# Optimization experiments

Measured on AMD Instinct MI355X. Metric: run time of the kernel, lower is better.

The kernel has to match this reference:

```python
import jax, jax.numpy as jnp
import numpy as np

N_NODES = 40000
N_EDGES = 640000
D_FEAT = 128
HIDDEN = 128
N_GRAPHS = 512


def setup_inputs() -> dict:
    key = jax.random.key(0)
    ks = jax.random.split(key, 6)
    x = jax.random.normal(ks[0], (N_NODES, D_FEAT), dtype=jnp.float32)
    edge_index = jax.random.randint(ks[1], (2, N_EDGES), 0, N_NODES, dtype=jnp.int32)
    batch = jnp.sort(jax.random.randint(ks[2], (N_NODES,), 0, N_GRAPHS, dtype=jnp.int32))
    s1 = 1.0 / np.sqrt(D_FEAT)
    s2 = 1.0 / np.sqrt(HIDDEN)
    W1 = jax.random.normal(ks[3], (D_FEAT, HIDDEN), dtype=jnp.float32) * s1
    b1 = jnp.zeros((HIDDEN,), dtype=jnp.float32)
    W2 = jax.random.normal(ks[4], (HIDDEN, HIDDEN), dtype=jnp.float32) * s2
    b2 = jnp.zeros((HIDDEN,), dtype=jnp.float32)
    Wfc = jax.random.normal(ks[5], (HIDDEN, 1), dtype=jnp.float32) * s2
    bfc = jnp.zeros((1,), dtype=jnp.float32)
    return {"x": x, "edge_index": edge_index, "batch": batch,
            "W1": W1, "b1": b1, "W2": W2, "b2": b2, "Wfc": Wfc, "bfc": bfc}


def _gcn_conv(x, edge_index, W, b):
    # PyG GCNConv: linear transform, add self-loops, symmetric deg^{-1/2} norm,
    # scatter-add messages from row (source) to col (target), then bias.
    n = x.shape[0]
    h = x @ W  # [N, H]
    row, col = edge_index[0], edge_index[1]
    ones = jnp.ones_like(col, dtype=h.dtype)
    deg = 1.0 + jax.ops.segment_sum(ones, col, num_segments=n)  # self-loop included
    dinv = jax.lax.rsqrt(deg)  # [N]
    norm = dinv[row] * dinv[col]  # [E]
    msg = h[row] * norm[:, None]  # [E, H]
    out = jax.ops.segment_sum(msg, col, num_segments=n)
    out = out + h * (dinv * dinv)[:, None]  # self-loop contribution
    return out + b


def _mean_pool(x, batch, num_graphs):
    sums = jax.ops.segment_sum(x, batch, num_segments=num_graphs)
    cnt = jax.ops.segment_sum(jnp.ones((x.shape[0],), dtype=x.dtype), batch, num_segments=num_graphs)
    return sums / jnp.maximum(cnt, 1.0)[:, None]


def reference(x, edge_index, batch, W1, b1, W2, b2, Wfc, bfc):
    h = jax.nn.relu(_gcn_conv(x, edge_index, W1, b1))
    h = jax.nn.relu(_gcn_conv(h, edge_index, W2, b2))
    g = _mean_pool(h, batch, N_GRAPHS)  # [G, H]
    return g @ Wfc + bfc  # [G, 1]
```

## Files before the change

kernel.cpp:

```cpp
#include <hip/hip_runtime.h>
#include <hip/hip_fp16.h>

#define N_NODES 40000
#define N_EDGES 640000
#define NFEAT   128
#define N_GRAPHS 512
#define SCAN_NB 157
#define EPAD_MAX (N_EDGES + 3 * N_NODES)


__global__ void edge_deg_int_kernel(const int* __restrict__ ei, int* __restrict__ degcnt, int E) {
    int e = blockIdx.x * blockDim.x + threadIdx.x;
    if (e < E) atomicAdd(&degcnt[ei[E + e]], 1);
}

__global__ void batch_hist_kernel(const int* __restrict__ batch, int* __restrict__ gcnt, int n) {
    int i = blockIdx.x * blockDim.x + threadIdx.x;
    if (i < n) atomicAdd(&gcnt[batch[i]], 1);
}

__global__ void dinv_from_int_kernel(const int* __restrict__ degcnt, float* __restrict__ dinv, int n) {
    int i = blockIdx.x * blockDim.x + threadIdx.x;
    if (i < n) dinv[i] = rsqrtf(1.0f + (float)degcnt[i]);
}

__global__ void scan1_kernel(const int* __restrict__ in, int* __restrict__ out,
                             int* __restrict__ bsums, float* __restrict__ dinv, int n) {
    __shared__ int tmp[256];
    int t = threadIdx.x;
    int i = blockIdx.x * 256 + t;
    int deg = (i < n) ? in[i] : 0;
    if (i < n) dinv[i] = rsqrtf(1.0f + (float)deg);
    int vp = (i < n) ? ((deg + 3) & ~3) : 0;
    tmp[t] = vp;
    __syncthreads();
    for (int off = 1; off < 256; off <<= 1) {
        int add = (t >= off) ? tmp[t - off] : 0;
        __syncthreads();
        tmp[t] += add;
        __syncthreads();
    }
    if (i < n) out[i] = tmp[t] - vp;
    if (t == 255) bsums[blockIdx.x] = tmp[255];
}

__global__ void scan2_kernel(int* __restrict__ bsums, int nb) {
    __shared__ int tmp[256];
    int t = threadIdx.x;
    int v = (t < nb) ? bsums[t] : 0;
    tmp[t] = v;
    __syncthreads();
    for (int off = 1; off < 256; off <<= 1) {
        int add = (t >= off) ? tmp[t - off] : 0;
        __syncthreads();
        tmp[t] += add;
        __syncthreads();
    }
    if (t < nb) bsums[t] = tmp[t] - v;
}

__global__ void scan3_kernel(int* __restrict__ rowptr, const int* __restrict__ bsums,
                             int* __restrict__ cursor, const int* __restrict__ degcnt,
                             int n) {
    int i = blockIdx.x * 256 + threadIdx.x;
    if (i < n) {
        int v = rowptr[i] + bsums[blockIdx.x];
        rowptr[i] = v;
        cursor[i] = v;
        if (i == n - 1) rowptr[n] = v + ((degcnt[i] + 3) & ~3);
    }
}

template <typename IdxT>
__global__ void fill_kernel(const int* __restrict__ ei, int* __restrict__ cursor,
                            IdxT* __restrict__ csr, int E) {
    int e = blockIdx.x * blockDim.x + threadIdx.x;
    if (e < E) {
        int c = ei[E + e];
        int p = atomicAdd(&cursor[c], 1);
        csr[p] = (IdxT)ei[e];
    }
}

template <typename IdxT>
__global__ void pad_kernel(const int* __restrict__ rowptr, const int* __restrict__ cursor,
                           IdxT* __restrict__ csr, int n) {
    int i = blockIdx.x * blockDim.x + threadIdx.x;
    if (i < n) {
        int end = rowptr[i + 1];
        for (int p = cursor[i]; p < end; ++p) csr[p] = (IdxT)N_NODES;
    }
}

__global__ void out_init_kernel(float* __restrict__ out, const float* __restrict__ bfc, int g) {
    int i = blockIdx.x * blockDim.x + threadIdx.x;
    if (i < g) out[i] = bfc[0];
}

template <typename OutT>
__global__ __launch_bounds__(256, 4) void gemm64_kernel(const float* __restrict__ X,
                                                        const float* __restrict__ W,
                                                        const float* __restrict__ dinv,
                                                        OutT* __restrict__ H) {
    __shared__ float Ws[128 * 64];
    const int colhalf = blockIdx.x & 1;
    const int tile    = blockIdx.x >> 1;

    for (int i = threadIdx.x; i < 2048; i += 256) {
        int k   = i >> 4;
        int cc4 = (i & 15) * 4;
        *(float4*)(Ws + k * 64 + cc4) = *(const float4*)(W + k * 128 + colhalf * 64 + cc4);
    }
    __syncthreads();

    const int rg = threadIdx.x >> 4;
    const int cg = threadIdx.x & 15;
    const int row0 = tile * 64 + rg * 4;
    const float* x0 = X + (size_t)row0 * NFEAT;

    float acc[4][4] = {};
    float4 xc[4], xn[4];
    #pragma unroll
    for (int i = 0; i < 4; i++) xc[i] = *(const float4*)(x0 + (size_t)i * NFEAT);

    #pragma unroll 4
    for (int k = 0; k < 128; k += 4) {
        const int kn = (k + 4) & 127;
        #pragma unroll
        for (int i = 0; i < 4; i++) xn[i] = *(const float4*)(x0 + (size_t)i * NFEAT + kn);

        float4 wv[4];
        #pragma unroll
        for (int m = 0; m < 4; m++) wv[m] = *(const float4*)(Ws + (k + m) * 64 + cg * 4);

        #pragma unroll
        for (int i = 0; i < 4; i++) {
            const float xi[4] = {xc[i].x, xc[i].y, xc[i].z, xc[i].w};
            #pragma unroll
            for (int m = 0; m < 4; m++) {
                acc[i][0] += xi[m] * wv[m].x;
                acc[i][1] += xi[m] * wv[m].y;
                acc[i][2] += xi[m] * wv[m].z;
                acc[i][3] += xi[m] * wv[m].w;
            }
        }
        #pragma unroll
        for (int i = 0; i < 4; i++) xc[i] = xn[i];
    }

    #pragma unroll
    for (int i = 0; i < 4; i++) {
        float dr = dinv[row0 + i];
        float v0 = acc[i][0] * dr, v1 = acc[i][1] * dr;
        float v2 = acc[i][2] * dr, v3 = acc[i][3] * dr;
        size_t off = (size_t)(row0 + i) * NFEAT + colhalf * 64 + cg * 4;
        if constexpr (sizeof(OutT) == 2) {
            __half2 p0 = __floats2half2_rn(v0, v1);
            __half2 p1 = __floats2half2_rn(v2, v3);
            uint2 pk;
            pk.x = *(unsigned int*)&p0;
            pk.y = *(unsigned int*)&p1;
            *(uint2*)((__half*)H + off) = pk;
        } else {
            float4 o = {v0, v1, v2, v3};
            *(float4*)((float*)H + off) = o;
        }
    }
}

__device__ inline float4 load_h4(const __half* p) {
    uint2 raw = *(const uint2*)p;
    __half2 h0 = *(__half2*)&raw.x;
    __half2 h1 = *(__half2*)&raw.y;
    float2 f0 = __half22float2(h0);
    float2 f1 = __half22float2(h1);
    return make_float4(f0.x, f0.y, f1.x, f1.y);
}

template <typename IdxT, typename IdxV, bool FUSE_POOL>
__global__ __launch_bounds__(256) void gather_h16_kernel(
        const int* __restrict__ rowptr, const IdxT* __restrict__ csr,
        const float* __restrict__ dinv, const __half* __restrict__ Ht,
        const float* __restrict__ bias, float* __restrict__ out,
        const float* __restrict__ Wfc, float* __restrict__ nodedot, int n) {
    int gid  = blockIdx.x * blockDim.x + threadIdx.x;
    int node = gid >> 6;
    if (node >= n) return;
    int lane = threadIdx.x & 63;
    int half = lane >> 5;
    int f4   = (lane & 31) * 4;

    int start = rowptr[node];
    int end   = rowptr[node + 1];

    float4 a0 = {0.f, 0.f, 0.f, 0.f};
    float4 a1 = {0.f, 0.f, 0.f, 0.f};
    if (half == 0) a0 = load_h4(Ht + (size_t)node * NFEAT + f4);

    for (int j = start; j < end; j += 4) {
        IdxV rr = *(const IdxV*)(csr + j);
        int r0 = half ? (int)rr.z : (int)rr.x;
        int r1 = half ? (int)rr.w : (int)rr.y;
        float4 v0 = load_h4(Ht + (size_t)r0 * NFEAT + f4);
        float4 v1 = load_h4(Ht + (size_t)r1 * NFEAT + f4);
        a0.x += v0.x; a0.y += v0.y; a0.z += v0.z; a0.w += v0.w;
        a1.x += v1.x; a1.y += v1.y; a1.z += v1.z; a1.w += v1.w;
    }
    a0.x += a1.x; a0.y += a1.y; a0.z += a1.z; a0.w += a1.w;

    a0.x += __shfl_xor(a0.x, 32, 64);
    a0.y += __shfl_xor(a0.y, 32, 64);
    a0.z += __shfl_xor(a0.z, 32, 64);
    a0.w += __shfl_xor(a0.w, 32, 64);

    if (half == 0) {
        float di  = dinv[node];
        float4 bb = *(const float4*)(bias + f4);
        float4 o;
        o.x = fmaxf(a0.x * di + bb.x, 0.0f);
        o.y = fmaxf(a0.y * di + bb.y, 0.0f);
        o.z = fmaxf(a0.z * di + bb.z, 0.0f);
        o.w = fmaxf(a0.w * di + bb.w, 0.0f);
        if (!FUSE_POOL) {
            *(float4*)(out + (size_t)node * NFEAT + f4) = o;
        } else {
            float4 wf = *(const float4*)(Wfc + f4);
            float d = o.x * wf.x + o.y * wf.y + o.z * wf.z + o.w * wf.w;
            d += __shfl_xor(d, 1, 64);
            d += __shfl_xor(d, 2, 64);
            d += __shfl_xor(d, 4, 64);
            d += __shfl_xor(d, 8, 64);
            d += __shfl_xor(d, 16, 64);
            if (lane == 0) nodedot[node] = d;
        }
    }
}

__global__ void pool_final_kernel(const float* __restrict__ nodedot,
                                  const int* __restrict__ batch,
                                  const int* __restrict__ gcnt,
                                  float* __restrict__ out, int n) {
    int i = blockIdx.x * blockDim.x + threadIdx.x;
    if (i < n) {
        int g = batch[i];
        int c = gcnt[g];
        float cf = (float)(c > 0 ? c : 1);
        atomicAdd(&out[g], nodedot[i] / cf);
    }
}

__global__ __launch_bounds__(256) void edge_scatter_kernel(const int* __restrict__ ei,
                                                           const float* __restrict__ dinv,
                                                           const float* __restrict__ H,
                                                           float* __restrict__ agg,
                                                           int E) {
    long long gid = (long long)blockIdx.x * blockDim.x + threadIdx.x;
    int e = (int)(gid >> 5);
    if (e >= E) return;
    int c4 = ((int)gid & 31) * 4;
    int r = ei[e];
    int c = ei[E + e];
    float norm = dinv[c];
    const float4 hv = *(const float4*)(H + (size_t)r * NFEAT + c4);
    float* dst = agg + (size_t)c * NFEAT + c4;
    atomicAdd(dst + 0, hv.x * norm);
    atomicAdd(dst + 1, hv.y * norm);
    atomicAdd(dst + 2, hv.z * norm);
    atomicAdd(dst + 3, hv.w * norm);
}

__global__ void post_kernel(float* __restrict__ agg, const float* __restrict__ H,
                            const float* __restrict__ dinv, const float* __restrict__ b,
                            int n) {
    int gid = blockIdx.x * blockDim.x + threadIdx.x;
    if (gid >= n * 32) return;
    int node = gid >> 5;
    int c4 = (gid & 31) * 4;
    float s = dinv[node];
    float4 a  = *(float4*)(agg + (size_t)gid * 4);
    float4 hv = *(const float4*)(H + (size_t)gid * 4);
    float4 bb = *(const float4*)(b + c4);
    float4 o;
    o.x = fmaxf(a.x + hv.x * s + bb.x, 0.0f);
    o.y = fmaxf(a.y + hv.y * s + bb.y, 0.0f);
    o.z = fmaxf(a.z + hv.z * s + bb.z, 0.0f);
    o.w = fmaxf(a.w + hv.w * s + bb.w, 0.0f);
    *(float4*)(agg + (size_t)gid * 4) = o;
}

__global__ __launch_bounds__(128) void pool_fc_kernel(const float* __restrict__ H,
                                                      const int* __restrict__ batch,
                                                      const float* __restrict__ Wfc,
                                                      const float* __restrict__ bfc,
                                                      float* __restrict__ out, int n) {
    int g = blockIdx.x;
    int tid = threadIdx.x;
    int lo = 0, hi = n;
    while (lo < hi) { int mid = (lo + hi) >> 1; if (batch[mid] < g) lo = mid + 1; else hi = mid; }
    int start = lo;
    hi = n;
    while (lo < hi) { int mid = (lo + hi) >> 1; if (batch[mid] < g + 1) lo = mid + 1; else hi = mid; }
    int end = lo;

    float acc = 0.0f;
    for (int nd = start; nd < end; ++nd) acc += H[(size_t)nd * NFEAT + tid];
    float cnt = (float)((end - start) > 0 ? (end - start) : 1);
    float v = (acc / cnt) * Wfc[tid];

    __shared__ float red[128];
    red[tid] = v;
    __syncthreads();
    #pragma unroll
    for (int s = 64; s > 0; s >>= 1) {
        if (tid < s) red[tid] += red[tid + s];
        __syncthreads();
    }
    if (tid == 0) out[g] = red[0] + bfc[0];
}

template <typename IdxT, typename IdxV>
static void run_csr_path(const float* x, const int* ei, const int* batch,
                         const float* W1, const float* b1, const float* W2,
                         const float* b2, const float* Wfc, const float* bfc,
                         float* out, void* d_ws, hipStream_t stream) {
    char* ws = (char*)d_ws;
    const size_t hbytes = (size_t)(N_NODES + 1) * NFEAT * sizeof(__half);
    const size_t obytes = (size_t)N_NODES * NFEAT * sizeof(float);
    __half* hbuf  = (__half*)ws;
    float*  obuf  = (float*)(ws + hbytes);
    IdxT*   csr   = (IdxT*)(ws + hbytes + obytes);
    char*   p     = ws + hbytes + obytes + ((size_t)EPAD_MAX * sizeof(IdxT) + 15) / 16 * 16;
    int*    rowptr = (int*)p;                p += ((size_t)(N_NODES + 1) * 4 + 15) / 16 * 16;
    float*  dinv   = (float*)p;              p += ((size_t)N_NODES * 4 + 15) / 16 * 16;
    int*    gcnt   = (int*)p;

    int* degcnt = (int*)obuf;
    int* cursor = (int*)obuf + N_NODES;
    int* bsums  = (int*)obuf + 2 * N_NODES;
    float* nodedot = (float*)obuf;

    hipMemsetAsync(degcnt, 0, (size_t)N_NODES * sizeof(int), stream);
    hipMemsetAsync(gcnt, 0, (size_t)N_GRAPHS * sizeof(int), stream);
    edge_deg_int_kernel<<<N_EDGES / 256, 256, 0, stream>>>(ei, degcnt, N_EDGES);
    batch_hist_kernel<<<SCAN_NB, 256, 0, stream>>>(batch, gcnt, N_NODES);
    scan1_kernel<<<SCAN_NB, 256, 0, stream>>>(degcnt, rowptr, bsums, dinv, N_NODES);
    scan2_kernel<<<1, 256, 0, stream>>>(bsums, SCAN_NB);
    scan3_kernel<<<SCAN_NB, 256, 0, stream>>>(rowptr, bsums, cursor, degcnt, N_NODES);
    fill_kernel<IdxT><<<N_EDGES / 256, 256, 0, stream>>>(ei, cursor, csr, N_EDGES);
    pad_kernel<IdxT><<<SCAN_NB, 256, 0, stream>>>(rowptr, cursor, csr, N_NODES);
    out_init_kernel<<<2, 256, 0, stream>>>(out, bfc, N_GRAPHS);
    hipMemsetAsync(hbuf + (size_t)N_NODES * NFEAT, 0, NFEAT * sizeof(__half), stream);

    gemm64_kernel<__half><<<(N_NODES / 64) * 2, 256, 0, stream>>>(x, W1, dinv, hbuf);
    gather_h16_kernel<IdxT, IdxV, false><<<(N_NODES * 64) / 256, 256, 0, stream>>>(
        rowptr, csr, dinv, hbuf, b1, obuf, nullptr, nullptr, N_NODES);

    gemm64_kernel<__half><<<(N_NODES / 64) * 2, 256, 0, stream>>>(obuf, W2, dinv, hbuf);
    gather_h16_kernel<IdxT, IdxV, true><<<(N_NODES * 64) / 256, 256, 0, stream>>>(
        rowptr, csr, dinv, hbuf, b2, nullptr, Wfc, nodedot, N_NODES);

    pool_final_kernel<<<SCAN_NB, 256, 0, stream>>>(nodedot, batch, gcnt, out, N_NODES);
}

extern "C" void kernel_launch(void* const* d_in, const int* in_sizes, int n_in,
                              void* d_out, int out_size, void* d_ws, size_t ws_size,
                              hipStream_t stream) {
    const float* x     = (const float*)d_in[0];
    const int*   ei    = (const int*)  d_in[1];
    const int*   batch = (const int*)  d_in[2];
    const float* W1    = (const float*)d_in[3];
    const float* b1    = (const float*)d_in[4];
    const float* W2    = (const float*)d_in[5];
    const float* b2    = (const float*)d_in[6];
    const float* Wfc   = (const float*)d_in[7];
    const float* bfc   = (const float*)d_in[8];
    float* out = (float*)d_out;

    const size_t hbytes = (size_t)(N_NODES + 1) * NFEAT * sizeof(__half);
    const size_t obytes = (size_t)N_NODES * NFEAT * sizeof(float);
    const size_t tail   = ((size_t)(N_NODES + 1) * 4 + 15) / 16 * 16
                        + ((size_t)N_NODES * 4 + 15) / 16 * 16
                        + (size_t)N_GRAPHS * 4;
    const size_t needA = hbytes + obytes + ((size_t)EPAD_MAX * 4 + 15) / 16 * 16 + tail;
    const size_t needB = hbytes + obytes + ((size_t)EPAD_MAX * 2 + 15) / 16 * 16 + tail;

    if (ws_size >= needA) {
        run_csr_path<int, int4>(x, ei, batch, W1, b1, W2, b2, Wfc, bfc, out, d_ws, stream);
    } else if (ws_size >= needB) {
        run_csr_path<unsigned short, ushort4>(x, ei, batch, W1, b1, W2, b2, Wfc, bfc, out, d_ws, stream);
    } else {
        float* ws   = (float*)d_ws;
        int*   degc = (int*)ws;
        float* dinv = ws + N_NODES;
        float* hbuf = ws + 2 * N_NODES;
        float* agg  = hbuf + (size_t)N_NODES * NFEAT;
        const size_t fb2 = (size_t)N_NODES * NFEAT * sizeof(float);

        hipMemsetAsync(degc, 0, (size_t)N_NODES * sizeof(int), stream);
        edge_deg_int_kernel<<<N_EDGES / 256, 256, 0, stream>>>(ei, degc, N_EDGES);
        dinv_from_int_kernel<<<SCAN_NB, 256, 0, stream>>>(degc, dinv, N_NODES);

        hipMemsetAsync(agg, 0, fb2, stream);
        gemm64_kernel<float><<<(N_NODES / 64) * 2, 256, 0, stream>>>(x, W1, dinv, hbuf);
        edge_scatter_kernel<<<(N_EDGES * 32) / 256, 256, 0, stream>>>(ei, dinv, hbuf, agg, N_EDGES);
        post_kernel<<<(N_NODES * 32) / 256, 256, 0, stream>>>(agg, hbuf, dinv, b1, N_NODES);

        gemm64_kernel<float><<<(N_NODES / 64) * 2, 256, 0, stream>>>(agg, W2, dinv, hbuf);
        hipMemsetAsync(agg, 0, fb2, stream);
        edge_scatter_kernel<<<(N_EDGES * 32) / 256, 256, 0, stream>>>(ei, dinv, hbuf, agg, N_EDGES);
        post_kernel<<<(N_NODES * 32) / 256, 256, 0, stream>>>(agg, hbuf, dinv, b2, N_NODES);

        pool_fc_kernel<<<N_GRAPHS, 128, 0, stream>>>(agg, batch, Wfc, bfc, out, N_NODES);
    }
}
```

Measured before the change: 324.5 us.

## Build CSR via two-pass bucketed binning with shared-memory atomics

Replaces the global-atomic degree count, fill and pad kernels with a two-level binning scheme. Edges are first binned by destination bucket (256 nodes each) using shared-memory histograms. Per-bucket kernels then compute degrees and dinv and scatter the CSR entries with shared-memory cursors. Several small init kernels and memsets are folded into one launch. This cuts random global atomics and improves locality, at the cost of an extra pass over the binned edges and a fixed per-bucket capacity (8192) that could overflow on skewed inputs.

After: 285.8 us. 1.14x faster.

```diff
diff --git a/kernel.cpp b/kernel.cpp
--- a/kernel.cpp
+++ b/kernel.cpp
@@ -6,12 +6,20 @@
 #define NFEAT   128
 #define N_GRAPHS 512
 #define SCAN_NB 157
+#define NBKT    157
+#define BKT_CAP 8192
+#define BIN_BLK_EDGES 2048
+#define NBLK_A ((N_EDGES + BIN_BLK_EDGES - 1) / BIN_BLK_EDGES)
 #define EPAD_MAX (N_EDGES + 3 * N_NODES)
 
-
-__global__ void edge_deg_int_kernel(const int* __restrict__ ei, int* __restrict__ degcnt, int E) {
-    int e = blockIdx.x * blockDim.x + threadIdx.x;
-    if (e < E) atomicAdd(&degcnt[ei[E + e]], 1);
+__global__ void init_misc_kernel(int* __restrict__ gcursor, int* __restrict__ gcnt,
+                                 float* __restrict__ out, const float* __restrict__ bfc,
+                                 __half* __restrict__ hsent) {
+    int t = threadIdx.x;
+    if (t < NBKT) gcursor[t] = 0;
+    float b = bfc[0];
+    for (int i = t; i < N_GRAPHS; i += 256) { gcnt[i] = 0; out[i] = b; }
+    if (t < NFEAT) hsent[t] = __float2half(0.0f);
 }
 
 __global__ void batch_hist_kernel(const int* __restrict__ batch, int* __restrict__ gcnt, int n) {
@@ -19,20 +27,68 @@
     if (i < n) atomicAdd(&gcnt[batch[i]], 1);
 }
 
-__global__ void dinv_from_int_kernel(const int* __restrict__ degcnt, float* __restrict__ dinv, int n) {
-    int i = blockIdx.x * blockDim.x + threadIdx.x;
-    if (i < n) dinv[i] = rsqrtf(1.0f + (float)degcnt[i]);
+__global__ __launch_bounds__(256) void bin_kernel(const int* __restrict__ ei,
+                                                  int* __restrict__ gcursor,
+                                                  unsigned int* __restrict__ binned) {
+    __shared__ int lhist[NBKT];
+    __shared__ int lbase[NBKT];
+    const int t  = threadIdx.x;
+    const int e0 = blockIdx.x * BIN_BLK_EDGES;
+
+    if (t < NBKT) lhist[t] = 0;
+    __syncthreads();
+
+    #pragma unroll
+    for (int i = 0; i < BIN_BLK_EDGES / 256; ++i) {
+        int e = e0 + i * 256 + t;
+        if (e < N_EDGES) atomicAdd(&lhist[ei[N_EDGES + e] >> 8], 1);
+    }
+    __syncthreads();
+
+    if (t < NBKT) { lbase[t] = atomicAdd(&gcursor[t], lhist[t]); lhist[t] = 0; }
+    __syncthreads();
+
+    #pragma unroll
+    for (int i = 0; i < BIN_BLK_EDGES / 256; ++i) {
+        int e = e0 + i * 256 + t;
+        if (e < N_EDGES) {
+            int c = ei[N_EDGES + e];
+            int r = ei[e];
+            int bkt = c >> 8;
+            int slot = atomicAdd(&lhist[bkt], 1);
+            binned[(size_t)bkt * BKT_CAP + lbase[bkt] + slot] =
+                (unsigned int)r | ((unsigned int)(c & 255) << 16);
+        }
+    }
+}
+
+__global__ __launch_bounds__(256) void bucket_hist_kernel(const unsigned int* __restrict__ binned,
+                                                          const int* __restrict__ gcursor,
+                                                          float* __restrict__ dinv,
+                                                          int* __restrict__ pdeg) {
+    __shared__ int chist[256];
+    const int b = blockIdx.x, t = threadIdx.x;
+    chist[t] = 0;
+    __syncthreads();
+    const int cnt = gcursor[b];
+    const unsigned int* src = binned + (size_t)b * BKT_CAP;
+    for (int i = t; i < cnt; i += 256) atomicAdd(&chist[src[i] >> 16], 1);
+    __syncthreads();
+    int col = b * 256 + t;
+    if (col < N_NODES) {
+        int d = chist[t];
+        dinv[col] = rsqrtf(1.0f + (float)d);
+        pdeg[col] = (d + 3) & ~3;
+    }
 }
 
 __global__ void scan1_kernel(const int* __restrict__ in, int* __restrict__ out,
-                             int* __restrict__ bsums, float* __restrict__ dinv, int n) {
+                             int* __restrict__ bsums, int n) {
     __shared__ int tmp[256];
     int t = threadIdx.x;
     int i = blockIdx.x * 256 + t;
-    int deg = (i < n) ? in[i] : 0;
-    if (i < n) dinv[i] = rsqrtf(1.0f + (float)deg);
-    int vp = (i < n) ? ((deg + 3) & ~3) : 0;
-    tmp[t] = vp;
+    int v = (i < n) ? in[i] : 0;
+    tmp[t] = v;
     __syncthreads();
     for (int off = 1; off < 256; off <<= 1) {
         int add = (t >= off) ? tmp[t - off] : 0;
@@ -40,7 +96,7 @@
         tmp[t] += add;
         __syncthreads();
     }
-    if (i < n) out[i] = tmp[t] - vp;
+    if (i < n) out[i] = tmp[t] - v;
     if (t == 255) bsums[blockIdx.x] = tmp[255];
 }
 
@@ -60,41 +116,37 @@
 }
 
 __global__ void scan3_kernel(int* __restrict__ rowptr, const int* __restrict__ bsums,
-                             int* __restrict__ cursor, const int* __restrict__ degcnt,
-                             int n) {
+                             const int* __restrict__ pdeg, int n) {
     int i = blockIdx.x * 256 + threadIdx.x;
     if (i < n) {
         int v = rowptr[i] + bsums[blockIdx.x];
         rowptr[i] = v;
-        cursor[i] = v;
-        if (i == n - 1) rowptr[n] = v + ((degcnt[i] + 3) & ~3);
+        if (i == n - 1) rowptr[n] = v + pdeg[i];
     }
 }
 
 template <typename IdxT>
-__global__ void fill_kernel(const int* __restrict__ ei, int* __restrict__ cursor,
-                            IdxT* __restrict__ csr, int E) {
-    int e = blockIdx.x * blockDim.x + threadIdx.x;
-    if (e < E) {
-        int c = ei[E + e];
-        int p = atomicAdd(&cursor[c], 1);
-        csr[p] = (IdxT)ei[e];
-    }
-}
-
-template <typename IdxT>
-__global__ void pad_kernel(const int* __restrict__ rowptr, const int* __restrict__ cursor,
-                           IdxT* __restrict__ csr, int n) {
-    int i = blockIdx.x * blockDim.x + threadIdx.x;
-    if (i < n) {
-        int end = rowptr[i + 1];
-        for (int p = cursor[i]; p < end; ++p) csr[p] = (IdxT)N_NODES;
-    }
-}
-
-__global__ void out_init_kernel(float* __restrict__ out, const float* __restrict__ bfc, int g) {
-    int i = blockIdx.x * blockDim.x + threadIdx.x;
-    if (i < g) out[i] = bfc[0];
+__global__ __launch_bounds__(256) void bucket_scatter_kernel(const unsigned int* __restrict__ binned,
+                                                             const int* __restrict__ gcursor,
+                                                             const int* __restrict__ rowptr,
+                                                             IdxT* __restrict__ csr) {
+    __shared__ int ccur[256];
+    const int b = blockIdx.x, t = threadIdx.x;
+    int col = b * 256 + t;
+    ccur[t] = (col < N_NODES) ? rowptr[col] : 0;
+    __syncthreads();
+    const int cnt = gcursor[b];
+    const unsigned int* src = binned + (size_t)b * BKT_CAP;
+    for (int i = t; i < cnt; i += 256) {
+        unsigned int u = src[i];
+        int slot = atomicAdd(&ccur[u >> 16], 1);
+        csr[slot] = (IdxT)(u & 0xFFFFu);
+    }
+    __syncthreads();
+    if (col < N_NODES) {
+        int end = rowptr[col + 1];
+        for (int p = ccur[t]; p < end; ++p) csr[p] = (IdxT)N_NODES;
+    }
 }
 
 template <typename OutT>
@@ -249,6 +301,16 @@
     }
 }
 
+__global__ void edge_deg_int_kernel(const int* __restrict__ ei, int* __restrict__ degcnt, int E) {
+    int e = blockIdx.x * blockDim.x + threadIdx.x;
+    if (e < E) atomicAdd(&degcnt[ei[E + e]], 1);
+}
+
+__global__ void dinv_from_int_kernel(const int* __restrict__ degcnt, float* __restrict__ dinv, int n) {
+    int i = blockIdx.x * blockDim.x + threadIdx.x;
+    if (i < n) dinv[i] = rsqrtf(1.0f + (float)degcnt[i]);
+}
+
 __global__ __launch_bounds__(256) void edge_scatter_kernel(const int* __restrict__ ei,
                                                            const float* __restrict__ dinv,
                                                            const float* __restrict__ H,
@@ -334,22 +396,21 @@
     float*  dinv   = (float*)p;              p += ((size_t)N_NODES * 4 + 15) / 16 * 16;
     int*    gcnt   = (int*)p;
 
-    int* degcnt = (int*)obuf;
-    int* cursor = (int*)obuf + N_NODES;
-    int* bsums  = (int*)obuf + 2 * N_NODES;
+    unsigned int* binned = (unsigned int*)obuf;
+    int* pdeg    = (int*)obuf + NBKT * BKT_CAP;
+    int* bsums   = pdeg + N_NODES;
+    int* gcursor = bsums + SCAN_NB;
     float* nodedot = (float*)obuf;
 
-    hipMemsetAsync(degcnt, 0, (size_t)N_NODES * sizeof(int), stream);
-    hipMemsetAsync(gcnt, 0, (size_t)N_GRAPHS * sizeof(int), stream);
-    edge_deg_int_kernel<<<N_EDGES / 256, 256, 0, stream>>>(ei, degcnt, N_EDGES);
+    init_misc_kernel<<<1, 256, 0, stream>>>(gcursor, gcnt, out, bfc,
+                                            hbuf + (size_t)N_NODES * NFEAT);
     batch_hist_kernel<<<SCAN_NB, 256, 0, stream>>>(batch, gcnt, N_NODES);
-    scan1_kernel<<<SCAN_NB, 256, 0, stream>>>(degcnt, rowptr, bsums, dinv, N_NODES);
+    bin_kernel<<<NBLK_A, 256, 0, stream>>>(ei, gcursor, binned);
+    bucket_hist_kernel<<<NBKT, 256, 0, stream>>>(binned, gcursor, dinv, pdeg);
+    scan1_kernel<<<SCAN_NB, 256, 0, stream>>>(pdeg, rowptr, bsums, N_NODES);
     scan2_kernel<<<1, 256, 0, stream>>>(bsums, SCAN_NB);
-    scan3_kernel<<<SCAN_NB, 256, 0, stream>>>(rowptr, bsums, cursor, degcnt, N_NODES);
-    fill_kernel<IdxT><<<N_EDGES / 256, 256, 0, stream>>>(ei, cursor, csr, N_EDGES);
-    pad_kernel<IdxT><<<SCAN_NB, 256, 0, stream>>>(rowptr, cursor, csr, N_NODES);
-    out_init_kernel<<<2, 256, 0, stream>>>(out, bfc, N_GRAPHS);
-    hipMemsetAsync(hbuf + (size_t)N_NODES * NFEAT, 0, NFEAT * sizeof(__half), stream);
+    scan3_kernel<<<SCAN_NB, 256, 0, stream>>>(rowptr, bsums, pdeg, N_NODES);
+    bucket_scatter_kernel<IdxT><<<NBKT, 256, 0, stream>>>(binned, gcursor, rowptr, csr);
 
     gemm64_kernel<__half><<<(N_NODES / 64) * 2, 256, 0, stream>>>(x, W1, dinv, hbuf);
     gather_h16_kernel<IdxT, IdxV, false><<<(N_NODES * 64) / 256, 256, 0, stream>>>(
```
